# Kernel tuning notes

Hardware: AMD Instinct MI355X
Metric: run time of the kernel (lower is better)

The kernel has to match this reference:

```python
import jax, jax.numpy as jnp
import numpy as np

N, X_DIM, Z_DIM, H = 4096, 256, 128, 512
NUM_ACTIONS = 4
TEMPERATURE = 0.1


def _init_linear(key, fan_in, fan_out):
    kw, kb = jax.random.split(key)
    bound = 1.0 / np.sqrt(fan_in)
    W = jax.random.uniform(kw, (fan_in, fan_out), minval=-bound, maxval=bound, dtype=jnp.float32)
    b = jax.random.uniform(kb, (fan_out,), minval=-bound, maxval=bound, dtype=jnp.float32)
    return W, b


def setup_inputs() -> dict:
    key = jax.random.key(0)
    ks = jax.random.split(key, 9)
    s = jax.random.normal(ks[0], (N, X_DIM), dtype=jnp.float32)
    sp = jax.random.normal(ks[1], (N, X_DIM), dtype=jnp.float32)
    a = jax.random.randint(ks[2], (N,), 0, NUM_ACTIONS)
    a1h = jax.nn.one_hot(a, NUM_ACTIONS, dtype=jnp.float32)
    # phi: x_dim -> 512 -> 512 -> z_dim
    pW0, pb0 = _init_linear(ks[3], X_DIM, H)
    pW1, pb1 = _init_linear(ks[4], H, H)
    pW2, pb2 = _init_linear(ks[5], H, Z_DIM)
    # g: x_dim + 4 -> 512 -> 512 -> z_dim
    gW0, gb0 = _init_linear(ks[6], X_DIM + NUM_ACTIONS, H)
    gW1, gb1 = _init_linear(ks[7], H, H)
    gW2, gb2 = _init_linear(ks[8], H, Z_DIM)
    return {"s": s, "sp": sp, "a1h": a1h,
            "pW0": pW0, "pb0": pb0, "pW1": pW1, "pb1": pb1, "pW2": pW2, "pb2": pb2,
            "gW0": gW0, "gb0": gb0, "gW1": gW1, "gb1": gb1, "gW2": gW2, "gb2": gb2}


def _mlp(x, W0, b0, W1, b1, W2, b2):
    h = jax.nn.relu(x @ W0 + b0)
    h = jax.nn.relu(h @ W1 + b1)
    return h @ W2 + b2


def reference(s, sp, a1h, pW0, pb0, pW1, pb1, pW2, pb2, gW0, gb0, gW1, gb1, gW2, gb2):
    z = _mlp(s, pW0, pb0, pW1, pb1, pW2, pb2)                      # [N, D]
    zpos = _mlp(jnp.concatenate([sp, a1h], axis=-1), gW0, gb0, gW1, gb1, gW2, gb2)  # [N, D]
    # -||z_i - zpos_j||^2 / T via the GEMM trick (avoids the [N,N,D] diff tensor)
    sq_z = jnp.sum(z * z, axis=-1, keepdims=True)                  # [N, 1]
    sq_p = jnp.sum(zpos * zpos, axis=-1)                            # [N]
    logits = -(sq_z + sq_p[None, :] - 2.0 * z @ zpos.T) / TEMPERATURE  # [N, N]
    # cross-entropy with targets = arange(N): diagonal is the positive
    log_probs = jax.nn.log_softmax(logits, axis=-1)
    loss = -jnp.mean(jnp.diagonal(log_probs))
    return loss
```

## Files before the change

kernel.cpp:

```cpp
#include <hip/hip_runtime.h>
#include <math.h>

#define NR 4096
#define ZD 128
#define HD 512
#define NJR 32
#define INV_T 10.0f

typedef __attribute__((ext_vector_type(8))) short bf16x8;
typedef __attribute__((ext_vector_type(4))) short short4v;
typedef __attribute__((ext_vector_type(4))) float f32x4;

__device__ __forceinline__ unsigned short f2bf(float f) {
  union { float f; unsigned u; } v; v.f = f;
  unsigned r = v.u + 0x7fff + ((v.u >> 16) & 1);
  return (unsigned short)(r >> 16);
}
__device__ __forceinline__ float bf2f(unsigned short b) {
  union { unsigned u; float f; } v; v.u = ((unsigned)b) << 16;
  return v.f;
}


__global__ __launch_bounds__(256) void prep(
    const float* __restrict__ s, const float* __restrict__ sp,
    const float* __restrict__ a1h,
    unsigned short* __restrict__ Sb, unsigned short* __restrict__ SPb,
    int* __restrict__ aidx,
    const float* __restrict__ pW0, unsigned short* __restrict__ pW0t,
    const float* __restrict__ pW1, unsigned short* __restrict__ pW1t,
    const float* __restrict__ pW2, unsigned short* __restrict__ pW2t,
    const float* __restrict__ gW0, unsigned short* __restrict__ gW0t,
    const float* __restrict__ gW1, unsigned short* __restrict__ gW1t,
    const float* __restrict__ gW2, unsigned short* __restrict__ gW2t,
    float* __restrict__ out) {
  int b = blockIdx.x, tid = threadIdx.x;
  if (b < 16) {
    int r = b * 256 + tid;
    int a = 0;
#pragma unroll
    for (int j = 0; j < 4; ++j) if (a1h[(size_t)r * 4 + j] > 0.5f) a = j;
    aidx[r] = a;
    if (b == 0 && tid == 0) out[0] = 0.f;
    return;
  }
  const int idx8 = tid & 127;
  const int h = idx8 & 1, p = idx8 >> 1, hi = p >> 4, l15 = p & 15;
  if (b < 2064) {
    const float* src = (b < 1040) ? s : sp;
    unsigned short* dst = (b < 1040) ? Sb : SPb;
    int lb = (b < 1040) ? b - 16 : b - 1040;
    int s0 = lb * 2 + (tid >> 7);
    int rf = s0 >> 3, ks = s0 & 7;
    int row = rf * 16 + l15, c0 = ks * 32 + hi * 4 + h * 16;
    float4 v = *(const float4*)&src[(size_t)row * 256 + c0];
    short4v o = { (short)f2bf(v.x), (short)f2bf(v.y), (short)f2bf(v.z), (short)f2bf(v.w) };
    *(short4v*)((char*)dst + (size_t)s0 * 1024 + idx8 * 8) = o;
    return;
  }
  int local = b - 2064;
  const float* W; unsigned short* Wt; int N, ksh;
  if (local < 128)      { W = pW0; Wt = pW0t; N = 512; ksh = 3; }
  else if (local < 384) { W = pW1; Wt = pW1t; N = 512; ksh = 4; local -= 128; }
  else if (local < 448) { W = pW2; Wt = pW2t; N = 128; ksh = 4; local -= 384; }
  else if (local < 576) { W = gW0; Wt = gW0t; N = 512; ksh = 3; local -= 448; }
  else if (local < 832) { W = gW1; Wt = gW1t; N = 512; ksh = 4; local -= 576; }
  else                  { W = gW2; Wt = gW2t; N = 128; ksh = 4; local -= 832; }
  int s0 = local * 2 + (tid >> 7);
  int rf = s0 >> ksh, ks = s0 & ((1 << ksh) - 1);
  int n = rf * 16 + l15, k0 = ks * 32 + hi * 4 + h * 16;
  short4v o = { (short)f2bf(W[(size_t)(k0 + 0) * N + n]),
                (short)f2bf(W[(size_t)(k0 + 1) * N + n]),
                (short)f2bf(W[(size_t)(k0 + 2) * N + n]),
                (short)f2bf(W[(size_t)(k0 + 3) * N + n]) };
  *(short4v*)((char*)Wt + (size_t)s0 * 1024 + idx8 * 8) = o;
}

template <bool RELU, bool GB, int FN, bool SQ>
__global__ __launch_bounds__(256) void gemm_fm(
    const unsigned short* __restrict__ A0, const unsigned short* __restrict__ A1,
    const unsigned short* __restrict__ W0, const unsigned short* __restrict__ W1,
    const float* __restrict__ b0, const float* __restrict__ b1,
    unsigned short* __restrict__ C0, unsigned short* __restrict__ C1,
    float* __restrict__ sqp2, int N, int K,
    const int* __restrict__ aidx, const float* __restrict__ gW0f) {
  const int tid = threadIdx.x, lane = tid & 63, w = tid >> 6;
  const int z = blockIdx.z;
  const char* Ab = (const char*)(z ? A1 : A0);
  const char* Wb = (const char*)(z ? W1 : W0);
  const float* bias = z ? b1 : b0;
  char* Cb = (char*)(z ? C1 : C0);
  const int KS = K >> 5;
  const int bm = blockIdx.x * 128 + w * 32;
  const int bn = blockIdx.y * (FN * 16);
  const int rowf = bm >> 4, colf = bn >> 4;
  const int lane16 = lane * 16;

  f32x4 acc[2][FN] = {};
#pragma unroll 4
  for (int ks = 0; ks < KS; ++ks) {
    bf16x8 af0 = *(const bf16x8*)(Ab + ((((size_t)rowf) * KS + ks) << 10) + lane16);
    bf16x8 af1 = *(const bf16x8*)(Ab + ((((size_t)rowf + 1) * KS + ks) << 10) + lane16);
    bf16x8 wf[FN];
#pragma unroll
    for (int fn = 0; fn < FN; ++fn)
      wf[fn] = *(const bf16x8*)(Wb + ((((size_t)colf + fn) * KS + ks) << 10) + lane16);
#pragma unroll
    for (int fn = 0; fn < FN; ++fn) {
      acc[0][fn] = __builtin_amdgcn_mfma_f32_16x16x32_bf16(wf[fn], af0, acc[0][fn], 0, 0, 0);
      acc[1][fn] = __builtin_amdgcn_mfma_f32_16x16x32_bf16(wf[fn], af1, acc[1][fn], 0, 0, 0);
    }
  }

  const int l15 = lane & 15, hi = lane >> 4;
  const int NS = N >> 5;
  float sq[2] = {0.f, 0.f};
  int ar[2];
  if (GB) {
    ar[0] = aidx[bm + l15];
    ar[1] = aidx[bm + 16 + l15];
  }
#pragma unroll
  for (int fm = 0; fm < 2; ++fm)
#pragma unroll
    for (int q = 0; q < FN / 2; ++q) {
      float4 bi0 = *(const float4*)&bias[bn + q * 32 + hi * 4];
      float4 bi1 = *(const float4*)&bias[bn + q * 32 + 16 + hi * 4];
      float v[8] = { acc[fm][2 * q][0] + bi0.x, acc[fm][2 * q][1] + bi0.y,
                     acc[fm][2 * q][2] + bi0.z, acc[fm][2 * q][3] + bi0.w,
                     acc[fm][2 * q + 1][0] + bi1.x, acc[fm][2 * q + 1][1] + bi1.y,
                     acc[fm][2 * q + 1][2] + bi1.z, acc[fm][2 * q + 1][3] + bi1.w };
      if (GB && z == 1) {
        float4 g0 = *(const float4*)&gW0f[(size_t)(256 + ar[fm]) * N + bn + q * 32 + hi * 4];
        float4 g1 = *(const float4*)&gW0f[(size_t)(256 + ar[fm]) * N + bn + q * 32 + 16 + hi * 4];
        v[0] += g0.x; v[1] += g0.y; v[2] += g0.z; v[3] += g0.w;
        v[4] += g1.x; v[5] += g1.y; v[6] += g1.z; v[7] += g1.w;
      }
      bf16x8 r;
#pragma unroll
      for (int i = 0; i < 8; ++i) {
        float vv = RELU ? fmaxf(v[i], 0.f) : v[i];
        unsigned short cv = f2bf(vv);
        r[i] = (short)cv;
        if (SQ) { float vb = bf2f(cv); sq[fm] += vb * vb; }
      }
      *(bf16x8*)(Cb + ((((size_t)rowf + fm) * NS + (bn >> 5) + q) << 10) + lane16) = r;
    }
  if (SQ && z == 1) {
#pragma unroll
    for (int fm = 0; fm < 2; ++fm) {
      float t = sq[fm];
      t += __shfl_xor(t, 16, 64);
      t += __shfl_xor(t, 32, 64);
      if (lane < 16) sqp2[(size_t)(bn >> 5) * NR + bm + fm * 16 + lane] = t;
    }
  }
}

__global__ __launch_bounds__(256) void logits_fm(
    const unsigned short* __restrict__ Zb, const unsigned short* __restrict__ Zpb,
    const float* __restrict__ sqp2, float* __restrict__ wm_,
    float* __restrict__ wsum, float* __restrict__ wdiag) {
  const int tid = threadIdx.x, lane = tid & 63, w = tid >> 6;
  const int l15 = lane & 15, hi4 = (lane >> 4) * 4;
  const int i0 = blockIdx.x * 64, jr = blockIdx.y;
  const int row16 = i0 + w * 16;
  const int jbase = jr * 128;
  const int lane16 = lane * 16;
  const char* Zc = (const char*)Zb;
  const char* Pc = (const char*)Zpb;
  const int rfA = row16 >> 4;

  bf16x8 afr[4];
#pragma unroll
  for (int ks = 0; ks < 4; ++ks)
    afr[ks] = *(const bf16x8*)(Zc + ((((size_t)rfA) * 4 + ks) << 10) + lane16);

  f32x4 acc[2][4] = {};
#pragma unroll
  for (int jt = 0; jt < 2; ++jt)
#pragma unroll
    for (int fn = 0; fn < 4; ++fn) {
      const int jf = (jbase >> 4) + jt * 4 + fn;
#pragma unroll
      for (int ks = 0; ks < 4; ++ks) {
        bf16x8 bfv = *(const bf16x8*)(Pc + ((((size_t)jf) * 4 + ks) << 10) + lane16);
        acc[jt][fn] = __builtin_amdgcn_mfma_f32_16x16x32_bf16(afr[ks], bfv, acc[jt][fn], 0, 0, 0);
      }
    }

  float spv[2][4];
#pragma unroll
  for (int jt = 0; jt < 2; ++jt)
#pragma unroll
    for (int fn = 0; fn < 4; ++fn) {
      int col = jbase + jt * 64 + fn * 16 + l15;
      spv[jt][fn] = sqp2[col] + sqp2[NR + col] + sqp2[2 * NR + col] + sqp2[3 * NR + col];
    }

#pragma unroll
  for (int e = 0; e < 4; ++e) {
    int grow = row16 + hi4 + e;
    float l[8], dd = 0.f;
    float mx = -INFINITY;
#pragma unroll
    for (int jt = 0; jt < 2; ++jt)
#pragma unroll
      for (int fn = 0; fn < 4; ++fn) {
        int col = jbase + jt * 64 + fn * 16 + l15;
        float lv = (2.f * acc[jt][fn][e] - spv[jt][fn]) * INV_T;
        l[jt * 4 + fn] = lv;
        mx = fmaxf(mx, lv);
        if (col == grow) dd = lv;
      }
#pragma unroll
    for (int off = 1; off < 16; off <<= 1) mx = fmaxf(mx, __shfl_xor(mx, off, 64));
    float sum = 0.f;
#pragma unroll
    for (int q = 0; q < 8; ++q) sum += __expf(l[q] - mx);
#pragma unroll
    for (int off = 1; off < 16; off <<= 1) sum += __shfl_xor(sum, off, 64);
    if (l15 == 0) {
      wm_[(size_t)jr * NR + grow] = mx;
      wsum[(size_t)jr * NR + grow] = sum;
    }
    if ((grow >> 7) == jr && l15 == (grow & 15)) wdiag[grow] = dd;
  }
}

__global__ __launch_bounds__(256) void finalize(const float* __restrict__ wm,
    const float* __restrict__ wsum, const float* __restrict__ wdiag,
    float* __restrict__ out) {
  int r = blockIdx.x * 256 + threadIdx.x;
  float mm = wm[r];
  float ss = wsum[r];
#pragma unroll
  for (int p = 1; p < NJR; ++p) {
    float mo = wm[(size_t)p * NR + r];
    float so = wsum[(size_t)p * NR + r];
    float mn = fmaxf(mm, mo);
    ss = ss * __expf(mm - mn) + so * __expf(mo - mn);
    mm = mn;
  }
  float loss_r = mm + logf(ss) - wdiag[r];
  float v = loss_r;
#pragma unroll
  for (int off = 32; off; off >>= 1) v += __shfl_xor(v, off, 64);
  __shared__ float partial[4];
  if ((threadIdx.x & 63) == 0) partial[threadIdx.x >> 6] = v;
  __syncthreads();
  if (threadIdx.x == 0)
    atomicAdd(out, (partial[0] + partial[1] + partial[2] + partial[3]) * (1.0f / (float)NR));
}

extern "C" void kernel_launch(void* const* d_in, const int* in_sizes, int n_in,
                              void* d_out, int out_size, void* d_ws, size_t ws_size,
                              hipStream_t stream) {
  const float* s   = (const float*)d_in[0];
  const float* sp  = (const float*)d_in[1];
  const float* a1h = (const float*)d_in[2];
  const float* pW0 = (const float*)d_in[3];
  const float* pb0 = (const float*)d_in[4];
  const float* pW1 = (const float*)d_in[5];
  const float* pb1 = (const float*)d_in[6];
  const float* pW2 = (const float*)d_in[7];
  const float* pb2 = (const float*)d_in[8];
  const float* gW0 = (const float*)d_in[9];
  const float* gb0 = (const float*)d_in[10];
  const float* gW1 = (const float*)d_in[11];
  const float* gb1 = (const float*)d_in[12];
  const float* gW2 = (const float*)d_in[13];
  const float* gb2 = (const float*)d_in[14];

  char* p = (char*)d_ws;
  unsigned short* Sb   = (unsigned short*)p; p += (size_t)NR * 256 * 2;
  unsigned short* SPb  = (unsigned short*)p; p += (size_t)NR * 256 * 2;
  unsigned short* H1   = (unsigned short*)p; p += (size_t)2 * NR * HD * 2;
  unsigned short* H2   = (unsigned short*)p; p += (size_t)2 * NR * HD * 2;
  unsigned short* Zall = (unsigned short*)p; p += (size_t)2 * NR * ZD * 2;
  unsigned short* pW0t = (unsigned short*)p; p += (size_t)256 * 512 * 2;
  unsigned short* pW1t = (unsigned short*)p; p += (size_t)512 * 512 * 2;
  unsigned short* pW2t = (unsigned short*)p; p += (size_t)512 * 128 * 2;
  unsigned short* gW0t = (unsigned short*)p; p += (size_t)256 * 512 * 2;
  unsigned short* gW1t = (unsigned short*)p; p += (size_t)512 * 512 * 2;
  unsigned short* gW2t = (unsigned short*)p; p += (size_t)512 * 128 * 2;
  float* sqp2 = (float*)p; p += (size_t)4 * NR * 4;
  float* wm   = (float*)p; p += (size_t)NJR * NR * 4;
  float* wsm  = (float*)p; p += (size_t)NJR * NR * 4;
  float* wdg  = (float*)p; p += (size_t)NR * 4;
  int*   aidx = (int*)p;  p += (size_t)NR * 4;

  unsigned short* H1g = H1 + (size_t)NR * HD;
  unsigned short* H2g = H2 + (size_t)NR * HD;
  unsigned short* Zb  = Zall;
  unsigned short* Zpb = Zall + (size_t)NR * ZD;

  dim3 blk(256);
  prep<<<2960, blk, 0, stream>>>(s, sp, a1h, Sb, SPb, aidx,
                                 pW0, pW0t, pW1, pW1t, pW2, pW2t,
                                 gW0, gW0t, gW1, gW1t, gW2, gW2t,
                                 (float*)d_out);

  gemm_fm<true, true, 4, false><<<dim3(32, 8, 2), blk, 0, stream>>>(
      Sb, SPb, pW0t, gW0t, pb0, gb0, H1, H1g, nullptr, 512, 256, aidx, gW0);
  gemm_fm<true, false, 4, false><<<dim3(32, 8, 2), blk, 0, stream>>>(
      H1, H1g, pW1t, gW1t, pb1, gb1, H2, H2g, nullptr, 512, 512, nullptr, nullptr);
  gemm_fm<false, false, 2, true><<<dim3(32, 4, 2), blk, 0, stream>>>(
      H2, H2g, pW2t, gW2t, pb2, gb2, Zb, Zpb, sqp2, 128, 512, nullptr, nullptr);

  logits_fm<<<dim3(NR / 64, NJR), blk, 0, stream>>>(Zb, Zpb, sqp2, wm, wsm, wdg);
  finalize<<<NR / 256, blk, 0, stream>>>(wm, wsm, wdg, (float*)d_out);
}
```

Before: 57.13 us.

## Stage GEMM and logits operands through LDS with double-buffered direct loads

Replaces the register-only fragment GEMM with a 128x128 block tile that stages A and W fragments into LDS using global_load_lds, double-buffered across K steps. Each wave computes a 64x64 sub-tile, so operands are reused more. The logits kernel now stages the 128-column Zpos slab in LDS and processes 128 rows per block. The aim is to cut redundant global/L2 fragment loads. In exchange, grid sizes drop (the last GEMM launches only 64 blocks) and barrier overhead is added.

```diff
diff --git a/kernel.cpp b/kernel.cpp
--- a/kernel.cpp
+++ b/kernel.cpp
@@ -10,6 +10,9 @@
 typedef __attribute__((ext_vector_type(8))) short bf16x8;
 typedef __attribute__((ext_vector_type(4))) short short4v;
 typedef __attribute__((ext_vector_type(4))) float f32x4;
+
+typedef const unsigned int __attribute__((address_space(1)))* gas_t;
+typedef unsigned int __attribute__((address_space(3)))* las_t;
 
 __device__ __forceinline__ unsigned short f2bf(float f) {
   union { float f; unsigned u; } v; v.f = f;
@@ -76,83 +79,123 @@
   *(short4v*)((char*)Wt + (size_t)s0 * 1024 + idx8 * 8) = o;
 }
 
-template <bool RELU, bool GB, int FN, bool SQ>
-__global__ __launch_bounds__(256) void gemm_fm(
+template <bool RELU, bool GB, bool SQ, int K>
+__global__ __launch_bounds__(256) void gemm_lds(
     const unsigned short* __restrict__ A0, const unsigned short* __restrict__ A1,
     const unsigned short* __restrict__ W0, const unsigned short* __restrict__ W1,
     const float* __restrict__ b0, const float* __restrict__ b1,
     unsigned short* __restrict__ C0, unsigned short* __restrict__ C1,
-    float* __restrict__ sqp2, int N, int K,
+    float* __restrict__ sqp2, int N,
     const int* __restrict__ aidx, const float* __restrict__ gW0f) {
+  __shared__ char As[2][16384];
+  __shared__ char Bs[2][16384];
+  constexpr int KS = K >> 5;
+  constexpr int NSTEP = K >> 6;
   const int tid = threadIdx.x, lane = tid & 63, w = tid >> 6;
+  const int wm = w >> 1, wn = w & 1;
   const int z = blockIdx.z;
   const char* Ab = (const char*)(z ? A1 : A0);
   const char* Wb = (const char*)(z ? W1 : W0);
   const float* bias = z ? b1 : b0;
   char* Cb = (char*)(z ? C1 : C0);
-  const int KS = K >> 5;
-  const int bm = blockIdx.x * 128 + w * 32;
-  const int bn = blockIdx.y * (FN * 16);
-  const int rowf = bm >> 4, colf = bn >> 4;
+  const int bm = blockIdx.x * 128, bn = blockIdx.y * 128;
   const int lane16 = lane * 16;
 
-  f32x4 acc[2][FN] = {};
-#pragma unroll 4
-  for (int ks = 0; ks < KS; ++ks) {
-    bf16x8 af0 = *(const bf16x8*)(Ab + ((((size_t)rowf) * KS + ks) << 10) + lane16);
-    bf16x8 af1 = *(const bf16x8*)(Ab + ((((size_t)rowf + 1) * KS + ks) << 10) + lane16);
-    bf16x8 wf[FN];
-#pragma unroll
-    for (int fn = 0; fn < FN; ++fn)
-      wf[fn] = *(const bf16x8*)(Wb + ((((size_t)colf + fn) * KS + ks) << 10) + lane16);
-#pragma unroll
-    for (int fn = 0; fn < FN; ++fn) {
-      acc[0][fn] = __builtin_amdgcn_mfma_f32_16x16x32_bf16(wf[fn], af0, acc[0][fn], 0, 0, 0);
-      acc[1][fn] = __builtin_amdgcn_mfma_f32_16x16x32_bf16(wf[fn], af1, acc[1][fn], 0, 0, 0);
-    }
+  const char* asrc[4];
+  const char* bsrc[4];
+#pragma unroll
+  for (int u = 0; u < 4; ++u) {
+    const int sl = w * 4 + u;
+    asrc[u] = Ab + (size_t)(((bm >> 4) + (sl >> 1)) * KS + (sl & 1)) * 1024 + lane16;
+    bsrc[u] = Wb + (size_t)(((bn >> 4) + (sl >> 1)) * KS + (sl & 1)) * 1024 + lane16;
+  }
+  auto stage = [&](int buf, int st) {
+    const int so = st * 2048;
+#pragma unroll
+    for (int u = 0; u < 4; ++u) {
+      const int sl = w * 4 + u;
+      __builtin_amdgcn_global_load_lds((gas_t)(asrc[u] + so), (las_t)&As[buf][sl * 1024], 16, 0, 0);
+      __builtin_amdgcn_global_load_lds((gas_t)(bsrc[u] + so), (las_t)&Bs[buf][sl * 1024], 16, 0, 0);
+    }
+  };
+
+  f32x4 acc[4][4] = {};
+  stage(0, 0);
+#pragma unroll
+  for (int st = 0; st < NSTEP; ++st) {
+    const int buf = st & 1;
+    if (st + 1 < NSTEP) {
+      stage(buf ^ 1, st + 1);
+      asm volatile("s_waitcnt vmcnt(8)" ::: "memory");
+    } else {
+      asm volatile("s_waitcnt vmcnt(0)" ::: "memory");
+    }
+    __builtin_amdgcn_s_barrier();
+    __builtin_amdgcn_sched_barrier(0);
+#pragma unroll
+    for (int kss = 0; kss < 2; ++kss) {
+      bf16x8 af[4], bfv[4];
+#pragma unroll
+      for (int i = 0; i < 4; ++i)
+        af[i] = *(const bf16x8*)(&As[buf][((wm * 4 + i) * 2 + kss) * 1024 + lane16]);
+#pragma unroll
+      for (int j = 0; j < 4; ++j)
+        bfv[j] = *(const bf16x8*)(&Bs[buf][((wn * 4 + j) * 2 + kss) * 1024 + lane16]);
+#pragma unroll
+      for (int i = 0; i < 4; ++i)
+#pragma unroll
+        for (int j = 0; j < 4; ++j)
+          acc[i][j] = __builtin_amdgcn_mfma_f32_16x16x32_bf16(bfv[j], af[i], acc[i][j], 0, 0, 0);
+    }
+    __builtin_amdgcn_sched_barrier(0);
+    __builtin_amdgcn_s_barrier();
   }
 
   const int l15 = lane & 15, hi = lane >> 4;
   const int NS = N >> 5;
-  float sq[2] = {0.f, 0.f};
-  int ar[2];
-  if (GB) {
-    ar[0] = aidx[bm + l15];
-    ar[1] = aidx[bm + 16 + l15];
-  }
-#pragma unroll
-  for (int fm = 0; fm < 2; ++fm)
-#pragma unroll
-    for (int q = 0; q < FN / 2; ++q) {
-      float4 bi0 = *(const float4*)&bias[bn + q * 32 + hi * 4];
-      float4 bi1 = *(const float4*)&bias[bn + q * 32 + 16 + hi * 4];
-      float v[8] = { acc[fm][2 * q][0] + bi0.x, acc[fm][2 * q][1] + bi0.y,
-                     acc[fm][2 * q][2] + bi0.z, acc[fm][2 * q][3] + bi0.w,
-                     acc[fm][2 * q + 1][0] + bi1.x, acc[fm][2 * q + 1][1] + bi1.y,
-                     acc[fm][2 * q + 1][2] + bi1.z, acc[fm][2 * q + 1][3] + bi1.w };
+  const int row0 = bm + wm * 64;
+  const int col0 = bn + wn * 64;
+  float sq[4] = {0.f, 0.f, 0.f, 0.f};
+  int ar[4] = {0, 0, 0, 0};
+  if (GB && z == 1) {
+#pragma unroll
+    for (int i = 0; i < 4; ++i) ar[i] = aidx[row0 + i * 16 + l15];
+  }
+#pragma unroll
+  for (int i = 0; i < 4; ++i) {
+    const int rfC = (row0 >> 4) + i;
+#pragma unroll
+    for (int q = 0; q < 2; ++q) {
+      float4 bi0 = *(const float4*)&bias[col0 + q * 32 + hi * 4];
+      float4 bi1 = *(const float4*)&bias[col0 + q * 32 + 16 + hi * 4];
+      float v[8] = { acc[i][2 * q][0] + bi0.x, acc[i][2 * q][1] + bi0.y,
+                     acc[i][2 * q][2] + bi0.z, acc[i][2 * q][3] + bi0.w,
+                     acc[i][2 * q + 1][0] + bi1.x, acc[i][2 * q + 1][1] + bi1.y,
+                     acc[i][2 * q + 1][2] + bi1.z, acc[i][2 * q + 1][3] + bi1.w };
       if (GB && z == 1) {
-        float4 g0 = *(const float4*)&gW0f[(size_t)(256 + ar[fm]) * N + bn + q * 32 + hi * 4];
-        float4 g1 = *(const float4*)&gW0f[(size_t)(256 + ar[fm]) * N + bn + q * 32 + 16 + hi * 4];
+        float4 g0 = *(const float4*)&gW0f[(size_t)(256 + ar[i]) * N + col0 + q * 32 + hi * 4];
+        float4 g1 = *(const float4*)&gW0f[(size_t)(256 + ar[i]) * N + col0 + q * 32 + 16 + hi * 4];
         v[0] += g0.x; v[1] += g0.y; v[2] += g0.z; v[3] += g0.w;
         v[4] += g1.x; v[5] += g1.y; v[6] += g1.z; v[7] += g1.w;
       }
       bf16x8 r;
 #pragma unroll
-      for (int i = 0; i < 8; ++i) {
-        float vv = RELU ? fmaxf(v[i], 0.f) : v[i];
+      for (int t = 0; t < 8; ++t) {
+        float vv = RELU ? fmaxf(v[t], 0.f) : v[t];
         unsigned short cv = f2bf(vv);
-        r[i] = (short)cv;
-        if (SQ) { float vb = bf2f(cv); sq[fm] += vb * vb; }
+        r[t] = (short)cv;
+        if (SQ) { float vb = bf2f(cv); sq[i] += vb * vb; }
       }
-      *(bf16x8*)(Cb + ((((size_t)rowf + fm) * NS + (bn >> 5) + q) << 10) + lane16) = r;
-    }
+      *(bf16x8*)(Cb + (size_t)(rfC * NS + ((col0 + q * 32) >> 5)) * 1024 + lane16) = r;
+    }
+  }
   if (SQ && z == 1) {
 #pragma unroll
-    for (int fm = 0; fm < 2; ++fm) {
-      float t = sq[fm];
+    for (int i = 0; i < 4; ++i) {
+      float t = sq[i];
       t += __shfl_xor(t, 16, 64);
       t += __shfl_xor(t, 32, 64);
-      if (lane < 16) sqp2[(size_t)(bn >> 5) * NR + bm + fm * 16 + lane] = t;
+      if (lane < 16) sqp2[(size_t)wn * NR + row0 + i * 16 + lane] = t;
     }
   }
 }
@@ -161,70 +204,84 @@
     const unsigned short* __restrict__ Zb, const unsigned short* __restrict__ Zpb,
     const float* __restrict__ sqp2, float* __restrict__ wm_,
     float* __restrict__ wsum, float* __restrict__ wdiag) {
+  __shared__ char Ps[32768];
   const int tid = threadIdx.x, lane = tid & 63, w = tid >> 6;
-  const int l15 = lane & 15, hi4 = (lane >> 4) * 4;
-  const int i0 = blockIdx.x * 64, jr = blockIdx.y;
-  const int row16 = i0 + w * 16;
+  const int l15 = lane & 15, hi = lane >> 4;
+  const int i0 = blockIdx.x * 128, jr = blockIdx.y;
+  const int row32 = i0 + w * 32;
   const int jbase = jr * 128;
   const int lane16 = lane * 16;
   const char* Zc = (const char*)Zb;
   const char* Pc = (const char*)Zpb;
-  const int rfA = row16 >> 4;
-
-  bf16x8 afr[4];
+
+  {
+    const char* src = Pc + (size_t)jbase * 256;
+#pragma unroll
+    for (int u = 0; u < 8; ++u) {
+      const int sl = w * 8 + u;
+      __builtin_amdgcn_global_load_lds((gas_t)(src + sl * 1024 + lane16),
+                                       (las_t)&Ps[sl * 1024], 16, 0, 0);
+    }
+  }
+  bf16x8 afr[2][4];
+#pragma unroll
+  for (int rf = 0; rf < 2; ++rf)
+#pragma unroll
+    for (int ks = 0; ks < 4; ++ks)
+      afr[rf][ks] = *(const bf16x8*)(Zc + (size_t)(((row32 >> 4) + rf) * 4 + ks) * 1024 + lane16);
+
+  asm volatile("s_waitcnt vmcnt(0)" ::: "memory");
+  __builtin_amdgcn_s_barrier();
+  __builtin_amdgcn_sched_barrier(0);
+
+  f32x4 acc[2][8] = {};
 #pragma unroll
   for (int ks = 0; ks < 4; ++ks)
-    afr[ks] = *(const bf16x8*)(Zc + ((((size_t)rfA) * 4 + ks) << 10) + lane16);
-
-  f32x4 acc[2][4] = {};
-#pragma unroll
-  for (int jt = 0; jt < 2; ++jt)
-#pragma unroll
-    for (int fn = 0; fn < 4; ++fn) {
-      const int jf = (jbase >> 4) + jt * 4 + fn;
-#pragma unroll
-      for (int ks = 0; ks < 4; ++ks) {
-        bf16x8 bfv = *(const bf16x8*)(Pc + ((((size_t)jf) * 4 + ks) << 10) + lane16);
-        acc[jt][fn] = __builtin_amdgcn_mfma_f32_16x16x32_bf16(afr[ks], bfv, acc[jt][fn], 0, 0, 0);
+#pragma unroll
+    for (int jf = 0; jf < 8; ++jf) {
+      bf16x8 bfv = *(const bf16x8*)(&Ps[(jf * 4 + ks) * 1024 + lane16]);
+      acc[0][jf] = __builtin_amdgcn_mfma_f32_16x16x32_bf16(bfv, afr[0][ks], acc[0][jf], 0, 0, 0);
+      acc[1][jf] = __builtin_amdgcn_mfma_f32_16x16x32_bf16(bfv, afr[1][ks], acc[1][jf], 0, 0, 0);
+    }
+
+  f32x4 spq[8];
+#pragma unroll
+  for (int jf = 0; jf < 8; ++jf) {
+    float4 s0 = *(const float4*)&sqp2[jbase + jf * 16 + hi * 4];
+    float4 s1 = *(const float4*)&sqp2[NR + jbase + jf * 16 + hi * 4];
+    spq[jf][0] = s0.x + s1.x; spq[jf][1] = s0.y + s1.y;
+    spq[jf][2] = s0.z + s1.z; spq[jf][3] = s0.w + s1.w;
+  }
+
+#pragma unroll
+  for (int rf = 0; rf < 2; ++rf) {
+    const int grow = row32 + rf * 16 + l15;
+    float mx = -INFINITY, dd = 0.f;
+    bool hasd = false;
+#pragma unroll
+    for (int jf = 0; jf < 8; ++jf)
+#pragma unroll
+      for (int e = 0; e < 4; ++e) {
+        const int j = jbase + jf * 16 + hi * 4 + e;
+        float lv = (2.f * acc[rf][jf][e] - spq[jf][e]) * INV_T;
+        acc[rf][jf][e] = lv;
+        mx = fmaxf(mx, lv);
+        if (j == grow) { dd = lv; hasd = true; }
       }
-    }
-
-  float spv[2][4];
-#pragma unroll
-  for (int jt = 0; jt < 2; ++jt)
-#pragma unroll
-    for (int fn = 0; fn < 4; ++fn) {
-      int col = jbase + jt * 64 + fn * 16 + l15;
-      spv[jt][fn] = sqp2[col] + sqp2[NR + col] + sqp2[2 * NR + col] + sqp2[3 * NR + col];
-    }
-
-#pragma unroll
-  for (int e = 0; e < 4; ++e) {
-    int grow = row16 + hi4 + e;
-    float l[8], dd = 0.f;
-    float mx = -INFINITY;
-#pragma unroll
-    for (int jt = 0; jt < 2; ++jt)
-#pragma unroll
-      for (int fn = 0; fn < 4; ++fn) {
-        int col = jbase + jt * 64 + fn * 16 + l15;
-        float lv = (2.f * acc[jt][fn][e] - spv[jt][fn]) * INV_T;
-        l[jt * 4 + fn] = lv;
-        mx = fmaxf(mx, lv);
-        if (col == grow) dd = lv;
-      }
-#pragma unroll
-    for (int off = 1; off < 16; off <<= 1) mx = fmaxf(mx, __shfl_xor(mx, off, 64));
+    mx = fmaxf(mx, __shfl_xor(mx, 16, 64));
+    mx = fmaxf(mx, __shfl_xor(mx, 32, 64));
     float sum = 0.f;
 #pragma unroll
-    for (int q = 0; q < 8; ++q) sum += __expf(l[q] - mx);
-#pragma unroll
-    for (int off = 1; off < 16; off <<= 1) sum += __shfl_xor(sum, off, 64);
-    if (l15 == 0) {
+    for (int jf = 0; jf < 8; ++jf)
+#pragma unroll
+      for (int e = 0; e < 4; ++e) sum += __expf(acc[rf][jf][e] - mx);
+    sum += __shfl_xor(sum, 16, 64);
+    sum += __shfl_xor(sum, 32, 64);
+    if (hi == 0) {
       wm_[(size_t)jr * NR + grow] = mx;
       wsum[(size_t)jr * NR + grow] = sum;
     }
-    if ((grow >> 7) == jr && l15 == (grow & 15)) wdiag[grow] = dd;
+    if (hasd) wdiag[grow] = dd;
   }
 }
 
@@ -301,13 +358,13 @@
                                  gW0, gW0t, gW1, gW1t, gW2, gW2t,
                                  (float*)d_out);
 
-  gemm_fm<true, true, 4, false><<<dim3(32, 8, 2), blk, 0, stream>>>(
-      Sb, SPb, pW0t, gW0t, pb0, gb0, H1, H1g, nullptr, 512, 256, aidx, gW0);
-  gemm_fm<true, false, 4, false><<<dim3(32, 8, 2), blk, 0, stream>>>(
-      H1, H1g, pW1t, gW1t, pb1, gb1, H2, H2g, nullptr, 512, 512, nullptr, nullptr);
-  gemm_fm<false, false, 2, true><<<dim3(32, 4, 2), blk, 0, stream>>>(
-      H2, H2g, pW2t, gW2t, pb2, gb2, Zb, Zpb, sqp2, 128, 512, nullptr, nullptr);
-
-  logits_fm<<<dim3(NR / 64, NJR), blk, 0, stream>>>(Zb, Zpb, sqp2, wm, wsm, wdg);
+  gemm_lds<true, true, false, 256><<<dim3(32, 4, 2), blk, 0, stream>>>(
+      Sb, SPb, pW0t, gW0t, pb0, gb0, H1, H1g, nullptr, 512, aidx, gW0);
+  gemm_lds<true, false, false, 512><<<dim3(32, 4, 2), blk, 0, stream>>>(
+      H1, H1g, pW1t, gW1t, pb1, gb1, H2, H2g, nullptr, 512, nullptr, nullptr);
+  gemm_lds<false, false, true, 512><<<dim3(32, 1, 2), blk, 0, stream>>>(
+      H2, H2g, pW2t, gW2t, pb2, gb2, Zb, Zpb, sqp2, 128, nullptr, nullptr);
+
+  logits_fm<<<dim3(NR / 128, NJR), blk, 0, stream>>>(Zb, Zpb, sqp2, wm, wsm, wdg);
   finalize<<<NR / 256, blk, 0, stream>>>(wm, wsm, wdg, (float*)d_out);
 }
```

New measurement: 56.40 us. No clear change (-1.3%).
